# Performance work log

Hardware: AMD Instinct MI355X
Metric: run time of the kernel (lower is better)

The kernel has to match this reference:

```python
import jax, jax.numpy as jnp
import numpy as np

K = 32  # neighbors per point (self.k)

def setup_inputs() -> dict:
    key = jax.random.key(0)
    k1, k2 = jax.random.split(key)
    B, N, C = 16, 4096, 64
    x = jax.random.normal(k1, (B, N, C), dtype=jnp.float32)
    idx = jax.random.randint(k2, (B, N, K), 0, N, dtype=jnp.int64)
    return {"x": x, "idx": idx}

def reference(x, idx):
    # pooled[b, n, :] = mean_k x[b, idx[b, n, k], :]
    # gather per-batch: xb[ib] -> [N, K, C]
    gathered = jax.vmap(lambda xb, ib: xb[ib])(x, idx)  # [B, N, K, C]
    return gathered.mean(axis=2)  # [B, N, C]
```

## Files before the change

kernel.cpp:

```cpp
#include <hip/hip_runtime.h>


#define BB 16
#define NN 4096
#define KK 32
#define CC 64

__global__ void detect_idx64_kernel(const int* __restrict__ w,
                                    int* __restrict__ flag) {
    int t = threadIdx.x;
    int v = w[2 * t + 1];
    unsigned long long nz = __ballot(v != 0);
    if (t == 0) *flag = (nz == 0ULL) ? 1 : 0;
}

__global__ __launch_bounds__(64)
void gapool_kernel(const float* __restrict__ x,
                   const int* __restrict__ idx32,
                   const int* __restrict__ flag,
                   float* __restrict__ out) {
    const int point = blockIdx.x;
    const int b = point >> 12;
    const int c = threadIdx.x;
    const int is64 = *flag;

    const float* __restrict__ xb = x + (size_t)b * NN * CC;

    float acc = 0.0f;
    if (is64) {
        const int* __restrict__ ip = idx32 + (size_t)point * KK * 2;
#pragma unroll
        for (int k = 0; k < KK; ++k) {
            const int j = ip[2 * k];
            acc += xb[(size_t)j * CC + c];
        }
    } else {
        const int* __restrict__ ip = idx32 + (size_t)point * KK;
#pragma unroll
        for (int k = 0; k < KK; ++k) {
            const int j = ip[k];
            acc += xb[(size_t)j * CC + c];
        }
    }

    out[(size_t)point * CC + c] = acc * (1.0f / KK);
}

extern "C" void kernel_launch(void* const* d_in, const int* in_sizes, int n_in,
                              void* d_out, int out_size, void* d_ws, size_t ws_size,
                              hipStream_t stream) {
    const float* x     = (const float*)d_in[0];
    const int*   idx32 = (const int*)d_in[1];
    float*       out   = (float*)d_out;
    int*         flag  = (int*)d_ws;

    detect_idx64_kernel<<<1, 64, 0, stream>>>(idx32, flag);

    gapool_kernel<<<BB * NN, 64, 0, stream>>>(x, idx32, flag, out);
}
```

Measured before the change: 95.55 us.

## Stage per-batch channel slices in LDS and gather with packed 16-bit indices

Adds a pre-pass that compresses indices to 16-bit values in workspace. The main kernel then loads a 4-channel slice of each batch's features into shared memory and performs the neighbor gathers from LDS with float4 reads. This replaces per-point blocks that gathered rows from global/L2. In exchange, index rows are re-read once per channel chunk, and random LDS access may cause bank conflicts with only one large block per CU.

```diff
diff --git a/kernel.cpp b/kernel.cpp
--- a/kernel.cpp
+++ b/kernel.cpp
@@ -5,45 +5,99 @@
 #define NN 4096
 #define KK 32
 #define CC 64
+#define CCH 4
+#define NCHUNK (CC / CCH)
+#define THREADS 512
 
-__global__ void detect_idx64_kernel(const int* __restrict__ w,
-                                    int* __restrict__ flag) {
-    int t = threadIdx.x;
-    int v = w[2 * t + 1];
-    unsigned long long nz = __ballot(v != 0);
-    if (t == 0) *flag = (nz == 0ULL) ? 1 : 0;
+__device__ __forceinline__ int detect_is64(const int* __restrict__ w) {
+    int v = w[2 * (threadIdx.x & 63) + 1];
+    return (__ballot(v != 0) == 0ULL) ? 1 : 0;
 }
 
-__global__ __launch_bounds__(64)
-void gapool_kernel(const float* __restrict__ x,
-                   const int* __restrict__ idx32,
-                   const int* __restrict__ flag,
-                   float* __restrict__ out) {
-    const int point = blockIdx.x;
-    const int b = point >> 12;
-    const int c = threadIdx.x;
-    const int is64 = *flag;
-
-    const float* __restrict__ xb = x + (size_t)b * NN * CC;
-
-    float acc = 0.0f;
+__global__ __launch_bounds__(256)
+void pack_idx_kernel(const int* __restrict__ idx32,
+                     ushort* __restrict__ out16) {
+    const int is64 = detect_is64(idx32);
+    const int tid = blockIdx.x * blockDim.x + threadIdx.x;
+    const int stride = gridDim.x * blockDim.x;
+    const int M = BB * NN * KK;
     if (is64) {
-        const int* __restrict__ ip = idx32 + (size_t)point * KK * 2;
-#pragma unroll
-        for (int k = 0; k < KK; ++k) {
-            const int j = ip[2 * k];
-            acc += xb[(size_t)j * CC + c];
+        const int4* __restrict__ in = (const int4*)idx32;
+        uint* __restrict__ o = (uint*)out16;
+        for (int i = tid; i < M / 2; i += stride) {
+            int4 v = in[i];
+            o[i] = (uint)(v.x & 0xFFFF) | ((uint)(v.z & 0xFFFF) << 16);
         }
     } else {
-        const int* __restrict__ ip = idx32 + (size_t)point * KK;
-#pragma unroll
-        for (int k = 0; k < KK; ++k) {
-            const int j = ip[k];
-            acc += xb[(size_t)j * CC + c];
+        const int4* __restrict__ in = (const int4*)idx32;
+        uint2* __restrict__ o = (uint2*)out16;
+        for (int i = tid; i < M / 4; i += stride) {
+            int4 v = in[i];
+            o[i] = make_uint2((uint)(v.x & 0xFFFF) | ((uint)(v.y & 0xFFFF) << 16),
+                              (uint)(v.z & 0xFFFF) | ((uint)(v.w & 0xFFFF) << 16));
         }
     }
+}
 
-    out[(size_t)point * CC + c] = acc * (1.0f / KK);
+__global__ __launch_bounds__(THREADS)
+void gapool_lds_kernel(const float* __restrict__ x,
+                       const ushort* __restrict__ idx16,
+                       float* __restrict__ out) {
+    __shared__ float4 tile[NN];
+
+    const int bid = blockIdx.x;
+    const int b = bid & 15;
+    const int chunk = bid >> 4;
+    const int c0 = chunk * CCH;
+
+    const float4* __restrict__ xb4 =
+        (const float4*)(x + ((size_t)b * NN) * CC + c0);
+    for (int n = threadIdx.x; n < NN; n += THREADS) {
+        tile[n] = xb4[(size_t)n * (CC / 4)];
+    }
+    __syncthreads();
+
+    const int wave = threadIdx.x >> 6;
+    const int lane = threadIdx.x & 63;
+    const int nwaves = THREADS >> 6;
+
+    const float s = 1.0f / KK;
+
+    for (int pg = wave; pg < NN / 64; pg += nwaves) {
+        const int n = pg * 64 + lane;
+        const size_t row = ((size_t)b * NN + n) * KK;
+
+        const uint4* __restrict__ ip = (const uint4*)(idx16 + row);
+        uint4 w0 = ip[0], w1 = ip[1], w2 = ip[2], w3 = ip[3];
+        uint p[8] = {w0.x, w0.y, w0.z, w0.w, w1.x, w1.y, w1.z, w1.w};
+        uint q[8] = {w2.x, w2.y, w2.z, w2.w, w3.x, w3.y, w3.z, w3.w};
+
+        float4 acc0 = make_float4(0.f, 0.f, 0.f, 0.f);
+        float4 acc1 = make_float4(0.f, 0.f, 0.f, 0.f);
+#pragma unroll
+        for (int i = 0; i < 8; ++i) {
+            {
+                float4 v = tile[p[i] & 0xFFFF];
+                acc0.x += v.x; acc0.y += v.y; acc0.z += v.z; acc0.w += v.w;
+            }
+            {
+                float4 v = tile[p[i] >> 16];
+                acc1.x += v.x; acc1.y += v.y; acc1.z += v.z; acc1.w += v.w;
+            }
+            {
+                float4 v = tile[q[i] & 0xFFFF];
+                acc0.x += v.x; acc0.y += v.y; acc0.z += v.z; acc0.w += v.w;
+            }
+            {
+                float4 v = tile[q[i] >> 16];
+                acc1.x += v.x; acc1.y += v.y; acc1.z += v.z; acc1.w += v.w;
+            }
+        }
+
+        float4 r = make_float4((acc0.x + acc1.x) * s, (acc0.y + acc1.y) * s,
+                               (acc0.z + acc1.z) * s, (acc0.w + acc1.w) * s);
+        *(float4*)(out + ((size_t)b * NN + n) * CC + c0) = r;
+    }
 }
 
 extern "C" void kernel_launch(void* const* d_in, const int* in_sizes, int n_in,
@@ -52,9 +106,9 @@
     const float* x     = (const float*)d_in[0];
     const int*   idx32 = (const int*)d_in[1];
     float*       out   = (float*)d_out;
-    int*         flag  = (int*)d_ws;
+    ushort*      idx16 = (ushort*)d_ws;
 
-    detect_idx64_kernel<<<1, 64, 0, stream>>>(idx32, flag);
+    pack_idx_kernel<<<2048, 256, 0, stream>>>(idx32, idx16);
 
-    gapool_kernel<<<BB * NN, 64, 0, stream>>>(x, idx32, flag, out);
+    gapool_lds_kernel<<<BB * NCHUNK, THREADS, 0, stream>>>(x, idx16, out);
 }
```

After: 90.51 us. 5.3% less time.
